# Optimization experiments

Measured on AMD Instinct MI355X. Metric: run time of the kernel, lower is better.

Reference implementation:

```python
import jax, jax.numpy as jnp
import numpy as np

N = 50000          # nodes
E = 1_600_000      # edges (avg degree 32)
IN = 128           # in_channels
H1, C1 = 4, 8      # conv1: heads=4, out=8 -> concat 32
OUT = 64           # out_channels (conv2, heads=1)
NEG_SLOPE = 0.2    # PyG GATConv default LeakyReLU slope


def _gat_layer(x, edge_index, W, att_src, att_dst, bias, heads, out_ch):
    """PyG-style GATConv (concat=True, add_self_loops=True).
    x: [N, F_in], edge_index: [2, E], W: [F_in, heads*out_ch],
    att_src/att_dst: [heads, out_ch], bias: [heads*out_ch].
    """
    n = x.shape[0]
    loops = jnp.arange(n)
    src = jnp.concatenate([edge_index[0], loops])  # message source j
    dst = jnp.concatenate([edge_index[1], loops])  # aggregation target i

    h = (x @ W).reshape(n, heads, out_ch)                 # [N, H, C]
    a_src = jnp.sum(h * att_src, axis=-1)                 # [N, H]
    a_dst = jnp.sum(h * att_dst, axis=-1)                 # [N, H]

    logits = jax.nn.leaky_relu(a_src[src] + a_dst[dst], NEG_SLOPE)  # [E', H]
    # segment softmax over incoming edges of each destination node
    m = jax.ops.segment_max(logits, dst, num_segments=n)            # [N, H]
    e = jnp.exp(logits - m[dst])
    s = jax.ops.segment_sum(e, dst, num_segments=n)                 # [N, H]
    alpha = e / (s[dst] + 1e-16)                                    # [E', H]

    msg = h[src] * alpha[..., None]                                 # [E', H, C]
    out = jax.ops.segment_sum(msg, dst, num_segments=n)             # [N, H, C]
    return out.reshape(n, heads * out_ch) + bias


def setup_inputs() -> dict:
    key = jax.random.key(0)
    ks = jax.random.split(key, 10)
    g = 0.1
    x = jax.random.normal(ks[0], (N, IN), jnp.float32)
    edge_index = jax.random.randint(ks[1], (2, E), 0, N, dtype=jnp.int64)
    W1 = jax.random.normal(ks[2], (IN, H1 * C1), jnp.float32) * g
    att_src1 = jax.random.normal(ks[3], (H1, C1), jnp.float32) * g
    att_dst1 = jax.random.normal(ks[4], (H1, C1), jnp.float32) * g
    b1 = jnp.zeros((H1 * C1,), jnp.float32)
    W2 = jax.random.normal(ks[5], (H1 * C1, OUT), jnp.float32) * g
    att_src2 = jax.random.normal(ks[6], (1, OUT), jnp.float32) * g
    att_dst2 = jax.random.normal(ks[7], (1, OUT), jnp.float32) * g
    b2 = jnp.zeros((OUT,), jnp.float32)
    return {"x": x, "edge_index": edge_index,
            "W1": W1, "att_src1": att_src1, "att_dst1": att_dst1, "b1": b1,
            "W2": W2, "att_src2": att_src2, "att_dst2": att_dst2, "b2": b2}


def reference(x, edge_index, W1, att_src1, att_dst1, b1, W2, att_src2, att_dst2, b2):
    h = _gat_layer(x, edge_index, W1, att_src1, att_dst1, b1, H1, C1)   # [N, 32]
    h = jax.nn.relu(h)
    out = _gat_layer(h, edge_index, W2, att_src2, att_dst2, b2, 1, OUT)  # [N, 64]
    return out
```

## Files before the change

### kernel.cpp

```cpp
#include <hip/hip_runtime.h>
#include <hip/hip_bf16.h>

#define IN_CH 128
#define H1C1  32
#define NH1   4
#define OUTC  64
#define NEG   0.2f
#define RPAD  8
#define BSH   6
#define BSZ   64
#define NBMAX 1024
#define CHUNK 4096
#define CAP   3072
#define PCAP  3584

typedef __hip_bfloat16 bf16;
typedef unsigned int u32;
typedef unsigned short u16;

__device__ __forceinline__ u16 f2bf_bits(float f) {
  bf16 v = __float2bfloat16(f);
  return *(u16*)&v;
}
__device__ __forceinline__ float bflo(u32 g) { return __uint_as_float(g << 16); }
__device__ __forceinline__ float bfhi(u32 g) { return __uint_as_float(g & 0xFFFF0000u); }


__global__ __launch_bounds__(256) void k_bin(
    const int* __restrict__ ei, int* __restrict__ bucket_fill,
    u32* __restrict__ data, int E, int n, int nb) {
  __shared__ int cnt[NBMAX];
  __shared__ int lbase[NBMAX];
  __shared__ int gbase[NBMAX];
  __shared__ u32 staged[CHUNK];
  int t = threadIdx.x;
  int lane = t & 63, wid = t >> 6;
  for (int b = t; b < nb; b += 256) cnt[b] = 0;
  __syncthreads();
  long base = (long)blockIdx.x * CHUNK;
  long totE = (long)E + n;
  u32 pk[CHUNK / 256];
  int bk[CHUNK / 256];
#pragma unroll
  for (int i = 0; i < CHUNK / 256; i++) {
    long e = base + i * 256 + t;
    if (e < totE) {
      int j, d;
      if (e < E) {
        j = ei[e]; d = ei[E + e];
        j = j < 0 ? 0 : (j >= n ? n - 1 : j);
        d = d < 0 ? 0 : (d >= n ? n - 1 : d);
      } else { j = d = (int)(e - E); }
      bk[i] = d >> BSH;
      pk[i] = ((u32)d << 16) | (u32)j;
      atomicAdd(&cnt[bk[i]], 1);
    } else bk[i] = -1;
  }
  __syncthreads();
  if (wid == 0) {
    int carry = 0;
    for (int b0 = 0; b0 < nb; b0 += 64) {
      int i = b0 + lane;
      int v = (i < nb) ? cnt[i] : 0;
      int orig = v;
      for (int off = 1; off < 64; off <<= 1) {
        int u = __shfl_up(v, off, 64);
        if (lane >= off) v += u;
      }
      if (i < nb) lbase[i] = carry + v - orig;
      carry += __shfl(v, 63, 64);
    }
  }
  __syncthreads();
  for (int b = t; b < nb; b += 256) {
    int c = cnt[b];
    gbase[b] = c ? atomicAdd(&bucket_fill[b], c) : 0;
    cnt[b] = 0;
  }
  __syncthreads();
#pragma unroll
  for (int i = 0; i < CHUNK / 256; i++) {
    if (bk[i] >= 0) {
      int loc = atomicAdd(&cnt[bk[i]], 1);
      staged[lbase[bk[i]] + loc] = pk[i];
    }
  }
  __syncthreads();
  long remL = totE - base;
  int rem = remL > CHUNK ? CHUNK : (int)remL;
  for (int idx = t; idx < rem; idx += 256) {
    u32 p = staged[idx];
    int b = (int)(p >> 16) >> BSH;
    int off2 = gbase[b] + (idx - lbase[b]);
    if (off2 < CAP) data[(size_t)b * CAP + off2] = p;
  }
}

__global__ __launch_bounds__(256) void k_bucket_scatter(
    const u32* __restrict__ data, const int* __restrict__ bucket_fill,
    int2* __restrict__ rowse, int* __restrict__ col, int n) {
  __shared__ int cur[BSZ];
  __shared__ int rp[BSZ];
  __shared__ int pd[BSZ];
  int t = threadIdx.x;
  int b = blockIdx.x;
  if (t < BSZ) cur[t] = 0;
  __syncthreads();
  int s = b * CAP;
  int cnt = bucket_fill[b];
  if (cnt > CAP) cnt = CAP;
  for (int i = t; i < cnt; i += 256)
    atomicAdd(&cur[(data[s + i] >> 16) & (BSZ - 1)], 1);
  __syncthreads();
  if (t < 64) {
    int raw = cur[t];
    int v = (raw + RPAD - 1) & ~(RPAD - 1);
    int orig = v;
    for (int off = 1; off < 64; off <<= 1) {
      int u = __shfl_up(v, off, 64);
      if (t >= off) v += u;
    }
    int r = b * PCAP + v - orig;
    rp[t] = r;
    pd[t] = orig;
    cur[t] = r;
    int node = (b << BSH) + t;
    if (node < n) rowse[node] = make_int2(r, r + orig);
  }
  __syncthreads();
  for (int i = t; i < cnt; i += 256) {
    u32 p = data[s + i];
    int dl = (int)(p >> 16) & (BSZ - 1);
    int pos = atomicAdd(&cur[dl], 1);
    col[pos] = (int)(p & 0xFFFFu);
  }
  __syncthreads();
  if (t < 64) {
    int c = cur[t];
    int end = rp[t] + pd[t];
    for (int k = c; k < end; k++) col[k] = n;
  }
}

__global__ __launch_bounds__(256) void k_l1_transform(
    const float* __restrict__ x, const float* __restrict__ W1,
    const float* __restrict__ as1, const float* __restrict__ ad1,
    u16* __restrict__ h1b, float* __restrict__ a_src, float* __restrict__ a_dst,
    int n) {
  __shared__ float W1s[32 * 128];
  __shared__ float xs[8 * IN_CH];
  int t = threadIdx.x;
  for (int idx = t; idx < IN_CH * H1C1; idx += 256) {
    int k = idx >> 5, m = idx & 31;
    W1s[(k >> 2) * 128 + m * 4 + (k & 3)] = W1[idx];
  }
  int base = blockIdx.x * 8;
  for (int idx = t; idx < 8 * IN_CH; idx += 256) {
    int row = idx >> 7, k = idx & 127;
    int nb = base + row;
    xs[idx] = (nb < n) ? x[(size_t)nb * IN_CH + k] : 0.f;
  }
  __syncthreads();
  int nl = t >> 5, m = t & 31;
  int node = base + nl;
  float acc = 0.f;
#pragma unroll
  for (int kg = 0; kg < 32; kg++) {
    float4 xv = *(const float4*)(xs + nl * IN_CH + kg * 4);
    float4 wv = *(const float4*)(W1s + kg * 128 + m * 4);
    acc += xv.x * wv.x + xv.y * wv.y + xv.z * wv.z + xv.w * wv.w;
  }
  float vs = acc * as1[m];
  float vd = acc * ad1[m];
  for (int off = 1; off < 8; off <<= 1) {
    vs += __shfl_xor(vs, off, 64);
    vd += __shfl_xor(vd, off, 64);
  }
  if (node < n) {
    h1b[node * H1C1 + m] = f2bf_bits(acc);
    if ((m & 7) == 0) {
      a_src[node * NH1 + (m >> 3)] = vs;
      a_dst[node * NH1 + (m >> 3)] = vd;
    }
  }
  if (blockIdx.x == 0) {
    if (t < H1C1) h1b[n * H1C1 + t] = 0;
    if (t < NH1)  a_src[n * NH1 + t] = -1e30f;
  }
}

__global__ __launch_bounds__(256) void k_l1_agg(
    const int2* __restrict__ rowse, const int* __restrict__ col,
    const u16* __restrict__ h1b, const float* __restrict__ a_src,
    const float* __restrict__ a_dst, const float* __restrict__ b1,
    const float* __restrict__ W2, const float* __restrict__ as2,
    const float* __restrict__ ad2,
    u16* __restrict__ h2, float* __restrict__ a_src2, float* __restrict__ a_dst2,
    int n) {
  __shared__ float W2s[8 * 256];
  __shared__ float hsh[16][H1C1];
  __shared__ int   js[4][64];
  __shared__ float wsh[4][NH1][68];
  int t = threadIdx.x;
  int wid = t >> 6, lane = t & 63;
  {
    int c = t & 63;
#pragma unroll
    for (int g = 0; g < 2; g++) {
      int kg = (t >> 6) + 4 * g;
      float4 v;
      v.x = W2[(kg * 4 + 0) * OUTC + c];
      v.y = W2[(kg * 4 + 1) * OUTC + c];
      v.z = W2[(kg * 4 + 2) * OUTC + c];
      v.w = W2[(kg * 4 + 3) * OUTC + c];
      *(float4*)(W2s + kg * 256 + c * 4) = v;
    }
  }
  int o = lane >> 3, u = lane & 7;
  int hd = u >> 1;
  for (int s = 0; s < 4; s++) {
    int node = blockIdx.x * 16 + wid * 4 + s;
    if (node >= n) continue;
    int2 se = rowse[node];
    int rs = se.x, re = se.y;
    float4 ad = *(const float4*)(a_dst + node * NH1);
    float a0 = 0.f, a1 = 0.f, a2 = 0.f, a3 = 0.f, sw = 0.f;
    for (int tb = rs; tb < re; tb += 64) {
      int kmax = re - tb; if (kmax > 64) kmax = 64;
      if (lane < kmax) {
        int j = col[tb + lane];
        float4 as = *(const float4*)(a_src + j * NH1);
        float l0 = as.x + ad.x; l0 = l0 > 0.f ? l0 : NEG * l0;
        float l1 = as.y + ad.y; l1 = l1 > 0.f ? l1 : NEG * l1;
        float l2 = as.z + ad.z; l2 = l2 > 0.f ? l2 : NEG * l2;
        float l3 = as.w + ad.w; l3 = l3 > 0.f ? l3 : NEG * l3;
        js[wid][lane] = j;
        wsh[wid][0][lane] = __expf(l0);
        wsh[wid][1][lane] = __expf(l1);
        wsh[wid][2][lane] = __expf(l2);
        wsh[wid][3][lane] = __expf(l3);
      }
      for (int k = 0; k < kmax; k += 8) {
        int j = js[wid][k + o];
        float wgt = wsh[wid][hd][k + o];
        uint2 g = *(const uint2*)(h1b + j * H1C1 + 4 * u);
        a0 += wgt * bflo(g.x);
        a1 += wgt * bfhi(g.x);
        a2 += wgt * bflo(g.y);
        a3 += wgt * bfhi(g.y);
        sw += wgt;
      }
    }
    for (int off = 8; off < 64; off <<= 1) {
      a0 += __shfl_xor(a0, off, 64);
      a1 += __shfl_xor(a1, off, 64);
      a2 += __shfl_xor(a2, off, 64);
      a3 += __shfl_xor(a3, off, 64);
      sw += __shfl_xor(sw, off, 64);
    }
    if (o == 0) {
      float inv = 1.f / (sw + 1e-16f);
      int c = 4 * u;
      hsh[wid * 4 + s][c]     = fmaxf(a0 * inv + b1[c], 0.f);
      hsh[wid * 4 + s][c + 1] = fmaxf(a1 * inv + b1[c + 1], 0.f);
      hsh[wid * 4 + s][c + 2] = fmaxf(a2 * inv + b1[c + 2], 0.f);
      hsh[wid * 4 + s][c + 3] = fmaxf(a3 * inv + b1[c + 3], 0.f);
    }
  }
  __syncthreads();
  float as2l = as2[lane], ad2l = ad2[lane];
  for (int r = 0; r < 4; r++) {
    int nl = wid * 4 + r;
    int node = blockIdx.x * 16 + nl;
    float acc = 0.f;
#pragma unroll
    for (int kg = 0; kg < 8; kg++) {
      float4 hv = *(const float4*)(&hsh[nl][kg * 4]);
      float4 wv = *(const float4*)(W2s + kg * 256 + lane * 4);
      acc += hv.x * wv.x + hv.y * wv.y + hv.z * wv.z + hv.w * wv.w;
    }
    float vs = acc * as2l;
    float vd = acc * ad2l;
    for (int off = 1; off < 64; off <<= 1) {
      vs += __shfl_xor(vs, off, 64);
      vd += __shfl_xor(vd, off, 64);
    }
    if (node < n) {
      h2[node * OUTC + lane] = f2bf_bits(acc);
      if (lane == 0) { a_src2[node] = vs; a_dst2[node] = vd; }
    }
  }
  if (blockIdx.x == 0) {
    if (t < OUTC) h2[n * OUTC + t] = 0;
    if (t == 0)   a_src2[n] = -1e30f;
  }
}

__global__ __launch_bounds__(256) void k_l2_agg(
    const int2* __restrict__ rowse, const int* __restrict__ col,
    const u16* __restrict__ h2, const float* __restrict__ a_src2,
    const float* __restrict__ a_dst2, const float* __restrict__ b2v,
    float* __restrict__ out, int n) {
  __shared__ int   js[4][64];
  __shared__ float wsh[4][64];
  int t = threadIdx.x;
  int wid = t >> 6, lane = t & 63;
  int o = lane >> 4, u = lane & 15;
  for (int s = 0; s < 4; s++) {
    int node = blockIdx.x * 16 + wid * 4 + s;
    if (node >= n) continue;
    int2 se = rowse[node];
    int rs = se.x, re = se.y;
    float ad = a_dst2[node];
    float a0 = 0.f, a1 = 0.f, a2 = 0.f, a3 = 0.f, sw = 0.f;
    for (int tb = rs; tb < re; tb += 64) {
      int kmax = re - tb; if (kmax > 64) kmax = 64;
      if (lane < kmax) {
        int j = col[tb + lane];
        float lg = a_src2[j] + ad;
        lg = lg > 0.f ? lg : NEG * lg;
        js[wid][lane] = j;
        wsh[wid][lane] = __expf(lg);
      }
      for (int k = 0; k < kmax; k += 4) {
        int j = js[wid][k + o];
        float wgt = wsh[wid][k + o];
        uint2 g = *(const uint2*)(h2 + j * OUTC + 4 * u);
        a0 += wgt * bflo(g.x);
        a1 += wgt * bfhi(g.x);
        a2 += wgt * bflo(g.y);
        a3 += wgt * bfhi(g.y);
        sw += wgt;
      }
    }
    for (int off = 16; off < 64; off <<= 1) {
      a0 += __shfl_xor(a0, off, 64);
      a1 += __shfl_xor(a1, off, 64);
      a2 += __shfl_xor(a2, off, 64);
      a3 += __shfl_xor(a3, off, 64);
      sw += __shfl_xor(sw, off, 64);
    }
    if (o == 0) {
      float inv = 1.f / (sw + 1e-16f);
      int c = 4 * u;
      float4 ov;
      ov.x = a0 * inv + b2v[c];
      ov.y = a1 * inv + b2v[c + 1];
      ov.z = a2 * inv + b2v[c + 2];
      ov.w = a3 * inv + b2v[c + 3];
      *(float4*)(out + node * OUTC + c) = ov;
    }
  }
}


extern "C" void kernel_launch(void* const* d_in, const int* in_sizes, int n_in,
                              void* d_out, int out_size, void* d_ws, size_t ws_size,
                              hipStream_t stream) {
  const float* x   = (const float*)d_in[0];
  const int*   ei  = (const int*)d_in[1];
  const float* W1  = (const float*)d_in[2];
  const float* as1 = (const float*)d_in[3];
  const float* ad1 = (const float*)d_in[4];
  const float* b1  = (const float*)d_in[5];
  const float* W2  = (const float*)d_in[6];
  const float* as2 = (const float*)d_in[7];
  const float* ad2 = (const float*)d_in[8];
  const float* b2  = (const float*)d_in[9];
  float* out = (float*)d_out;

  int n = in_sizes[0] / IN_CH;
  int E = in_sizes[1] / 2;
  int nb = (n + BSZ - 1) >> BSH;
  long tot = (long)E + n;
  int nA = (int)((tot + CHUNK - 1) / CHUNK);

  char* w = (char*)d_ws;
  auto al = [](size_t v) { return (v + 255) & ~(size_t)255; };
  size_t off = 0;
  int*  bucket_fill = (int*)(w + off);  off += al((size_t)nb * 4);
  int2* rowse       = (int2*)(w + off); off += al((size_t)(n + 1) * 8);
  u32*  data        = (u32*)(w + off);  off += al((size_t)nb * CAP * 4);
  int*  col         = (int*)(w + off);  off += al((size_t)nb * PCAP * 4);
  u16*  h1b         = (u16*)(w + off);  off += al((size_t)(n + 1) * H1C1 * 2);
  float* a_src1     = (float*)(w + off); off += al((size_t)(n + 1) * NH1 * 4);
  float* a_dst1     = (float*)(w + off); off += al((size_t)(n + 1) * NH1 * 4);
  u16*  h2          = (u16*)(w + off);  off += al((size_t)(n + 1) * OUTC * 2);
  float* a_src2     = (float*)(w + off); off += al((size_t)(n + 1) * 4);
  float* a_dst2     = (float*)(w + off); off += al((size_t)(n + 1) * 4);

  hipMemsetAsync(bucket_fill, 0, (size_t)nb * 4, stream);
  hipLaunchKernelGGL(k_bin, dim3(nA), dim3(256), 0, stream,
                     ei, bucket_fill, data, E, n, nb);
  hipLaunchKernelGGL(k_bucket_scatter, dim3(nb), dim3(256), 0, stream,
                     data, bucket_fill, rowse, col, n);

  hipLaunchKernelGGL(k_l1_transform, dim3((n + 7) / 8), dim3(256), 0, stream,
                     x, W1, as1, ad1, h1b, a_src1, a_dst1, n);
  hipLaunchKernelGGL(k_l1_agg, dim3((n + 15) / 16), dim3(256), 0, stream,
                     rowse, col, h1b, a_src1, a_dst1, b1,
                     W2, as2, ad2, h2, a_src2, a_dst2, n);

  hipLaunchKernelGGL(k_l2_agg, dim3((n + 15) / 16), dim3(256), 0, stream,
                     rowse, col, h2, a_src2, a_dst2, b2, out, n);
}
```

Before: 236.1 us.

## Fuse edge binning with layer-1 transform and unroll aggregation gathers

Merges the edge bucketing kernel and the layer-1 linear transform into one launch, with block ranges choosing which job to run, so the two independent stages overlap and one launch is removed. The neighbor gather loops in both aggregation kernels are unrolled to issue 2 or 4 independent loads per iteration for more memory-level parallelism. Row padding is raised to 16 (and column capacity enlarged) so the wider unrolled loops stay within padded, zero-weight entries. This costs more padded edges and memory.

After: 211.6 us. 10.4% less time.

```diff
diff --git a/kernel.cpp b/kernel.cpp
--- a/kernel.cpp
+++ b/kernel.cpp
@@ -6,13 +6,13 @@
 #define NH1   4
 #define OUTC  64
 #define NEG   0.2f
-#define RPAD  8
+#define RPAD  16
 #define BSH   6
 #define BSZ   64
 #define NBMAX 1024
 #define CHUNK 4096
 #define CAP   3072
-#define PCAP  3584
+#define PCAP  4096
 
 typedef __hip_bfloat16 bf16;
 typedef unsigned int u32;
@@ -25,74 +25,119 @@
 __device__ __forceinline__ float bflo(u32 g) { return __uint_as_float(g << 16); }
 __device__ __forceinline__ float bfhi(u32 g) { return __uint_as_float(g & 0xFFFF0000u); }
 
-
-__global__ __launch_bounds__(256) void k_bin(
+__global__ __launch_bounds__(256) void k_bin_tr(
     const int* __restrict__ ei, int* __restrict__ bucket_fill,
-    u32* __restrict__ data, int E, int n, int nb) {
-  __shared__ int cnt[NBMAX];
-  __shared__ int lbase[NBMAX];
-  __shared__ int gbase[NBMAX];
-  __shared__ u32 staged[CHUNK];
+    u32* __restrict__ data, int E, int n, int nb, int nA,
+    const float* __restrict__ x, const float* __restrict__ W1,
+    const float* __restrict__ as1, const float* __restrict__ ad1,
+    u16* __restrict__ h1b, float* __restrict__ a_src, float* __restrict__ a_dst) {
+  __shared__ __align__(16) char smem[28672];
   int t = threadIdx.x;
-  int lane = t & 63, wid = t >> 6;
-  for (int b = t; b < nb; b += 256) cnt[b] = 0;
-  __syncthreads();
-  long base = (long)blockIdx.x * CHUNK;
-  long totE = (long)E + n;
-  u32 pk[CHUNK / 256];
-  int bk[CHUNK / 256];
+  if ((int)blockIdx.x < nA) {
+    int* cnt   = (int*)smem;
+    int* lbase = cnt + NBMAX;
+    int* gbase = lbase + NBMAX;
+    u32* staged = (u32*)(gbase + NBMAX);
+    int lane = t & 63, wid = t >> 6;
+    for (int b = t; b < nb; b += 256) cnt[b] = 0;
+    __syncthreads();
+    long base = (long)blockIdx.x * CHUNK;
+    long totE = (long)E + n;
+    u32 pk[CHUNK / 256];
+    int bk[CHUNK / 256];
 #pragma unroll
-  for (int i = 0; i < CHUNK / 256; i++) {
-    long e = base + i * 256 + t;
-    if (e < totE) {
-      int j, d;
-      if (e < E) {
-        j = ei[e]; d = ei[E + e];
-        j = j < 0 ? 0 : (j >= n ? n - 1 : j);
-        d = d < 0 ? 0 : (d >= n ? n - 1 : d);
-      } else { j = d = (int)(e - E); }
-      bk[i] = d >> BSH;
-      pk[i] = ((u32)d << 16) | (u32)j;
-      atomicAdd(&cnt[bk[i]], 1);
-    } else bk[i] = -1;
-  }
-  __syncthreads();
-  if (wid == 0) {
-    int carry = 0;
-    for (int b0 = 0; b0 < nb; b0 += 64) {
-      int i = b0 + lane;
-      int v = (i < nb) ? cnt[i] : 0;
-      int orig = v;
-      for (int off = 1; off < 64; off <<= 1) {
-        int u = __shfl_up(v, off, 64);
-        if (lane >= off) v += u;
-      }
-      if (i < nb) lbase[i] = carry + v - orig;
-      carry += __shfl(v, 63, 64);
-    }
-  }
-  __syncthreads();
-  for (int b = t; b < nb; b += 256) {
-    int c = cnt[b];
-    gbase[b] = c ? atomicAdd(&bucket_fill[b], c) : 0;
-    cnt[b] = 0;
-  }
-  __syncthreads();
+    for (int i = 0; i < CHUNK / 256; i++) {
+      long e = base + i * 256 + t;
+      if (e < totE) {
+        int j, d;
+        if (e < E) {
+          j = ei[e]; d = ei[E + e];
+          j = j < 0 ? 0 : (j >= n ? n - 1 : j);
+          d = d < 0 ? 0 : (d >= n ? n - 1 : d);
+        } else { j = d = (int)(e - E); }
+        bk[i] = d >> BSH;
+        pk[i] = ((u32)d << 16) | (u32)j;
+        atomicAdd(&cnt[bk[i]], 1);
+      } else bk[i] = -1;
+    }
+    __syncthreads();
+    if (wid == 0) {
+      int carry = 0;
+      for (int b0 = 0; b0 < nb; b0 += 64) {
+        int i = b0 + lane;
+        int v = (i < nb) ? cnt[i] : 0;
+        int orig = v;
+        for (int off = 1; off < 64; off <<= 1) {
+          int u = __shfl_up(v, off, 64);
+          if (lane >= off) v += u;
+        }
+        if (i < nb) lbase[i] = carry + v - orig;
+        carry += __shfl(v, 63, 64);
+      }
+    }
+    __syncthreads();
+    for (int b = t; b < nb; b += 256) {
+      int c = cnt[b];
+      gbase[b] = c ? atomicAdd(&bucket_fill[b], c) : 0;
+      cnt[b] = 0;
+    }
+    __syncthreads();
 #pragma unroll
-  for (int i = 0; i < CHUNK / 256; i++) {
-    if (bk[i] >= 0) {
-      int loc = atomicAdd(&cnt[bk[i]], 1);
-      staged[lbase[bk[i]] + loc] = pk[i];
-    }
-  }
-  __syncthreads();
-  long remL = totE - base;
-  int rem = remL > CHUNK ? CHUNK : (int)remL;
-  for (int idx = t; idx < rem; idx += 256) {
-    u32 p = staged[idx];
-    int b = (int)(p >> 16) >> BSH;
-    int off2 = gbase[b] + (idx - lbase[b]);
-    if (off2 < CAP) data[(size_t)b * CAP + off2] = p;
+    for (int i = 0; i < CHUNK / 256; i++) {
+      if (bk[i] >= 0) {
+        int loc = atomicAdd(&cnt[bk[i]], 1);
+        staged[lbase[bk[i]] + loc] = pk[i];
+      }
+    }
+    __syncthreads();
+    long remL = totE - base;
+    int rem = remL > CHUNK ? CHUNK : (int)remL;
+    for (int idx = t; idx < rem; idx += 256) {
+      u32 p = staged[idx];
+      int b = (int)(p >> 16) >> BSH;
+      int off2 = gbase[b] + (idx - lbase[b]);
+      if (off2 < CAP) data[(size_t)b * CAP + off2] = p;
+    }
+  } else {
+    float* W1s = (float*)smem;
+    float* xs  = W1s + 32 * 128;
+    for (int idx = t; idx < IN_CH * H1C1; idx += 256) {
+      int k = idx >> 5, m = idx & 31;
+      W1s[(k >> 2) * 128 + m * 4 + (k & 3)] = W1[idx];
+    }
+    int base = (blockIdx.x - nA) * 8;
+    for (int idx = t; idx < 8 * IN_CH; idx += 256) {
+      int row = idx >> 7, k = idx & 127;
+      int nb2 = base + row;
+      xs[idx] = (nb2 < n) ? x[(size_t)nb2 * IN_CH + k] : 0.f;
+    }
+    __syncthreads();
+    int nl = t >> 5, m = t & 31;
+    int node = base + nl;
+    float acc = 0.f;
+#pragma unroll
+    for (int kg = 0; kg < 32; kg++) {
+      float4 xv = *(const float4*)(xs + nl * IN_CH + kg * 4);
+      float4 wv = *(const float4*)(W1s + kg * 128 + m * 4);
+      acc += xv.x * wv.x + xv.y * wv.y + xv.z * wv.z + xv.w * wv.w;
+    }
+    float vs = acc * as1[m];
+    float vd = acc * ad1[m];
+    for (int off = 1; off < 8; off <<= 1) {
+      vs += __shfl_xor(vs, off, 64);
+      vd += __shfl_xor(vd, off, 64);
+    }
+    if (node < n) {
+      h1b[node * H1C1 + m] = f2bf_bits(acc);
+      if ((m & 7) == 0) {
+        a_src[node * NH1 + (m >> 3)] = vs;
+        a_dst[node * NH1 + (m >> 3)] = vd;
+      }
+    }
+    if ((int)blockIdx.x == nA) {
+      if (t < H1C1) h1b[n * H1C1 + t] = 0;
+      if (t < NH1)  a_src[n * NH1 + t] = -1e30f;
+    }
   }
 }
 
@@ -139,53 +184,6 @@
     int c = cur[t];
     int end = rp[t] + pd[t];
     for (int k = c; k < end; k++) col[k] = n;
-  }
-}
-
-__global__ __launch_bounds__(256) void k_l1_transform(
-    const float* __restrict__ x, const float* __restrict__ W1,
-    const float* __restrict__ as1, const float* __restrict__ ad1,
-    u16* __restrict__ h1b, float* __restrict__ a_src, float* __restrict__ a_dst,
-    int n) {
-  __shared__ float W1s[32 * 128];
-  __shared__ float xs[8 * IN_CH];
-  int t = threadIdx.x;
-  for (int idx = t; idx < IN_CH * H1C1; idx += 256) {
-    int k = idx >> 5, m = idx & 31;
-    W1s[(k >> 2) * 128 + m * 4 + (k & 3)] = W1[idx];
-  }
-  int base = blockIdx.x * 8;
-  for (int idx = t; idx < 8 * IN_CH; idx += 256) {
-    int row = idx >> 7, k = idx & 127;
-    int nb = base + row;
-    xs[idx] = (nb < n) ? x[(size_t)nb * IN_CH + k] : 0.f;
-  }
-  __syncthreads();
-  int nl = t >> 5, m = t & 31;
-  int node = base + nl;
-  float acc = 0.f;
-#pragma unroll
-  for (int kg = 0; kg < 32; kg++) {
-    float4 xv = *(const float4*)(xs + nl * IN_CH + kg * 4);
-    float4 wv = *(const float4*)(W1s + kg * 128 + m * 4);
-    acc += xv.x * wv.x + xv.y * wv.y + xv.z * wv.z + xv.w * wv.w;
-  }
-  float vs = acc * as1[m];
-  float vd = acc * ad1[m];
-  for (int off = 1; off < 8; off <<= 1) {
-    vs += __shfl_xor(vs, off, 64);
-    vd += __shfl_xor(vd, off, 64);
-  }
-  if (node < n) {
-    h1b[node * H1C1 + m] = f2bf_bits(acc);
-    if ((m & 7) == 0) {
-      a_src[node * NH1 + (m >> 3)] = vs;
-      a_dst[node * NH1 + (m >> 3)] = vd;
-    }
-  }
-  if (blockIdx.x == 0) {
-    if (t < H1C1) h1b[n * H1C1 + t] = 0;
-    if (t < NH1)  a_src[n * NH1 + t] = -1e30f;
   }
 }
 
@@ -240,15 +238,18 @@
         wsh[wid][2][lane] = __expf(l2);
         wsh[wid][3][lane] = __expf(l3);
       }
-      for (int k = 0; k < kmax; k += 8) {
-        int j = js[wid][k + o];
-        float wgt = wsh[wid][hd][k + o];
-        uint2 g = *(const uint2*)(h1b + j * H1C1 + 4 * u);
-        a0 += wgt * bflo(g.x);
-        a1 += wgt * bfhi(g.x);
-        a2 += wgt * bflo(g.y);
-        a3 += wgt * bfhi(g.y);
-        sw += wgt;
+      for (int k = 0; k < kmax; k += 16) {
+        int j0 = js[wid][k + o];
+        int j1 = js[wid][k + 8 + o];
+        float w0 = wsh[wid][hd][k + o];
+        float w1 = wsh[wid][hd][k + 8 + o];
+        uint2 g0 = *(const uint2*)(h1b + j0 * H1C1 + 4 * u);
+        uint2 g1 = *(const uint2*)(h1b + j1 * H1C1 + 4 * u);
+        a0 += w0 * bflo(g0.x) + w1 * bflo(g1.x);
+        a1 += w0 * bfhi(g0.x) + w1 * bfhi(g1.x);
+        a2 += w0 * bflo(g0.y) + w1 * bflo(g1.y);
+        a3 += w0 * bfhi(g0.y) + w1 * bfhi(g1.y);
+        sw += w0 + w1;
       }
     }
     for (int off = 8; off < 64; off <<= 1) {
@@ -322,15 +323,28 @@
         js[wid][lane] = j;
         wsh[wid][lane] = __expf(lg);
       }
-      for (int k = 0; k < kmax; k += 4) {
-        int j = js[wid][k + o];
-        float wgt = wsh[wid][k + o];
-        uint2 g = *(const uint2*)(h2 + j * OUTC + 4 * u);
-        a0 += wgt * bflo(g.x);
-        a1 += wgt * bfhi(g.x);
-        a2 += wgt * bflo(g.y);
-        a3 += wgt * bfhi(g.y);
-        sw += wgt;
+      for (int k = 0; k < kmax; k += 16) {
+        int j0 = js[wid][k + o];
+        int j1 = js[wid][k + 4 + o];
+        int j2 = js[wid][k + 8 + o];
+        int j3 = js[wid][k + 12 + o];
+        float w0 = wsh[wid][k + o];
+        float w1 = wsh[wid][k + 4 + o];
+        float w2 = wsh[wid][k + 8 + o];
+        float w3 = wsh[wid][k + 12 + o];
+        uint2 g0 = *(const uint2*)(h2 + j0 * OUTC + 4 * u);
+        uint2 g1 = *(const uint2*)(h2 + j1 * OUTC + 4 * u);
+        uint2 g2 = *(const uint2*)(h2 + j2 * OUTC + 4 * u);
+        uint2 g3 = *(const uint2*)(h2 + j3 * OUTC + 4 * u);
+        a0 += w0 * bflo(g0.x) + w1 * bflo(g1.x);
+        a0 += w2 * bflo(g2.x) + w3 * bflo(g3.x);
+        a1 += w0 * bfhi(g0.x) + w1 * bfhi(g1.x);
+        a1 += w2 * bfhi(g2.x) + w3 * bfhi(g3.x);
+        a2 += w0 * bflo(g0.y) + w1 * bflo(g1.y);
+        a2 += w2 * bflo(g2.y) + w3 * bflo(g3.y);
+        a3 += w0 * bfhi(g0.y) + w1 * bfhi(g1.y);
+        a3 += w2 * bfhi(g2.y) + w3 * bfhi(g3.y);
+        sw += (w0 + w1) + (w2 + w3);
       }
     }
     for (int off = 16; off < 64; off <<= 1) {
@@ -374,6 +388,7 @@
   int nb = (n + BSZ - 1) >> BSH;
   long tot = (long)E + n;
   int nA = (int)((tot + CHUNK - 1) / CHUNK);
+  int nTr = (n + 7) / 8;
 
   char* w = (char*)d_ws;
   auto al = [](size_t v) { return (v + 255) & ~(size_t)255; };
@@ -390,13 +405,12 @@
   float* a_dst2     = (float*)(w + off); off += al((size_t)(n + 1) * 4);
 
   hipMemsetAsync(bucket_fill, 0, (size_t)nb * 4, stream);
-  hipLaunchKernelGGL(k_bin, dim3(nA), dim3(256), 0, stream,
-                     ei, bucket_fill, data, E, n, nb);
+  hipLaunchKernelGGL(k_bin_tr, dim3(nA + nTr), dim3(256), 0, stream,
+                     ei, bucket_fill, data, E, n, nb, nA,
+                     x, W1, as1, ad1, h1b, a_src1, a_dst1);
   hipLaunchKernelGGL(k_bucket_scatter, dim3(nb), dim3(256), 0, stream,
                      data, bucket_fill, rowse, col, n);
 
-  hipLaunchKernelGGL(k_l1_transform, dim3((n + 7) / 8), dim3(256), 0, stream,
-                     x, W1, as1, ad1, h1b, a_src1, a_dst1, n);
   hipLaunchKernelGGL(k_l1_agg, dim3((n + 15) / 16), dim3(256), 0, stream,
                      rowse, col, h1b, a_src1, a_dst1, b1,
                      W2, as2, ad2, h2, a_src2, a_dst2, n);
```
